# Kernel tuning notes

Measured on AMD Instinct MI355X. Metric: run time of the kernel, lower is better.

## Reference

```python
import jax, jax.numpy as jnp
import numpy as np

N_NODES = 60000
N_EDGES = 960000
IN_C = 128
HID = 4 * IN_C       # 512
D_CAT = 8 * IN_C     # 1024
D_FC = 16 * IN_C     # 2048
D_L1 = 32 * IN_C     # 4096
OUT_C = 64
BN_EPS = 1e-5
LEAKY_SLOPE = 0.01


def setup_inputs() -> dict:
    key = jax.random.key(0)
    ks = jax.random.split(key, 32)
    d = {}
    d['x'] = jax.random.normal(ks[0], (N_NODES, IN_C), dtype=jnp.float32)
    d['edge_index'] = jax.random.randint(ks[1], (2, N_EDGES), 0, N_NODES, dtype=jnp.int64)

    def lin(k, fan_in, fan_out):
        k1, k2 = jax.random.split(k)
        bound = 1.0 / np.sqrt(fan_in)
        w = jax.random.uniform(k1, (fan_in, fan_out), jnp.float32, -bound, bound)
        b = jax.random.uniform(k2, (fan_out,), jnp.float32, -bound, bound)
        return w, b

    # GIN conv A MLP: Linear(IN_C,HID) -> BN(HID) -> ReLU -> Linear(HID,HID) -> ReLU
    d['w1a'], d['b1a'] = lin(ks[2], IN_C, HID)
    d['gamma_a'] = jnp.ones((HID,), jnp.float32)
    d['beta_a'] = jnp.zeros((HID,), jnp.float32)
    d['mean_a'] = jax.random.normal(ks[3], (HID,), jnp.float32) * 0.1
    d['var_a'] = jax.random.uniform(ks[4], (HID,), jnp.float32, 0.5, 1.5)
    d['w2a'], d['b2a'] = lin(ks[5], HID, HID)
    # GIN conv B MLP
    d['w1b'], d['b1b'] = lin(ks[6], IN_C, HID)
    d['gamma_b'] = jnp.ones((HID,), jnp.float32)
    d['beta_b'] = jnp.zeros((HID,), jnp.float32)
    d['mean_b'] = jax.random.normal(ks[7], (HID,), jnp.float32) * 0.1
    d['var_b'] = jax.random.uniform(ks[8], (HID,), jnp.float32, 0.5, 1.5)
    d['w2b'], d['b2b'] = lin(ks[9], HID, HID)
    # dense head
    d['fc_w'], d['fc_b'] = lin(ks[10], D_CAT, D_FC)
    d['l1_w'], d['l1_b'] = lin(ks[11], D_FC, D_L1)
    d['l2_w'], d['l2_b'] = lin(ks[12], D_L1, D_FC)
    d['out_w'], d['out_b'] = lin(ks[13], D_FC, OUT_C)
    return d


def _gin_conv(x, edge_index, w1, b1, gamma, beta, mean, var, w2, b2):
    # GINConv, eps=0: h_i = MLP(x_i + sum_{j->i} x_j)
    src, dst = edge_index[0], edge_index[1]
    agg = jax.ops.segment_sum(x[src], dst, num_segments=x.shape[0])
    h = x + agg
    h = h @ w1 + b1
    # BatchNorm1d in eval mode (running stats)
    h = (h - mean) * jax.lax.rsqrt(var + BN_EPS) * gamma + beta
    h = jax.nn.relu(h)
    h = jax.nn.relu(h @ w2 + b2)
    return h


def reference(x, edge_index, w1a, b1a, gamma_a, beta_a, mean_a, var_a, w2a, b2a,
              w1b, b1b, gamma_b, beta_b, mean_b, var_b, w2b, b2b,
              fc_w, fc_b, l1_w, l1_b, l2_w, l2_b, out_w, out_b):
    x1 = _gin_conv(x, edge_index, w1a, b1a, gamma_a, beta_a, mean_a, var_a, w2a, b2a)
    x2 = _gin_conv(x, edge_index, w1b, b1b, gamma_b, beta_b, mean_b, var_b, w2b, b2b)
    h = jnp.concatenate([x1, x2], axis=1)               # [N, 8*in]
    h = jax.nn.leaky_relu(h @ fc_w + fc_b, LEAKY_SLOPE)  # dropout is identity in eval
    h = h @ l1_w + l1_b
    h = h @ l2_w + l2_b
    h = jax.nn.sigmoid(h @ out_w + out_b)
    return h
```

## Files before the change

### kernel.cpp

```cpp
#include <hip/hip_runtime.h>


#define NN 60000
#define NE 960000
#define C_IN 128
#define HID 512
#define DCAT 1024
#define DFC 2048
#define DL1 4096
#define OUTC 64

typedef __bf16 bf16x8 __attribute__((ext_vector_type(8)));
typedef float floatx4 __attribute__((ext_vector_type(4)));

__device__ __forceinline__ unsigned short f2b(float f) {
  unsigned int u = __float_as_uint(f);
  unsigned int r = (u + 0x7fffu + ((u >> 16) & 1u)) >> 16;
  return (unsigned short)r;
}

#define GLOAD_LDS16(g, l)                                                     \
  __builtin_amdgcn_global_load_lds(                                           \
      (__attribute__((address_space(1))) void*)(g),                           \
      (__attribute__((address_space(3))) void*)(l), 16, 0, 0)

__global__ void k_bnparams(const float* __restrict__ g,
                           const float* __restrict__ be,
                           const float* __restrict__ mn,
                           const float* __restrict__ vr,
                           const float* __restrict__ b1,
                           float* __restrict__ scale, float* __restrict__ shift) {
  int i = blockIdx.x * 256 + threadIdx.x;
  if (i < HID) {
    float s = g[i] * rsqrtf(vr[i] + 1e-5f);
    scale[i] = s;
    shift[i] = (b1[i] - mn[i]) * s + be[i];
  }
}

__global__ void k_transpose(const float* __restrict__ in,
                            unsigned short* __restrict__ out, int K, int N) {
  __shared__ float t[32][33];
  int n0 = blockIdx.x * 32, k0 = blockIdx.y * 32;
  int tx = threadIdx.x & 31, ty = threadIdx.x >> 5;
#pragma unroll
  for (int i = 0; i < 32; i += 8)
    t[ty + i][tx] = in[(size_t)(k0 + ty + i) * N + n0 + tx];
  __syncthreads();
#pragma unroll
  for (int i = 0; i < 32; i += 8)
    out[(size_t)(n0 + ty + i) * K + k0 + tx] = f2b(t[tx][ty + i]);
}

__global__ void k_deg(const int* __restrict__ dst, int* __restrict__ deg) {
  int e = blockIdx.x * 256 + threadIdx.x;
  if (e < NE) atomicAdd(&deg[dst[e]], 1);
}

__global__ void k_scan1(const int* __restrict__ deg, int* __restrict__ offs,
                        int* __restrict__ bsum) {
  __shared__ int t[256];
  int i = blockIdx.x * 256 + threadIdx.x;
  int v = (i < NN) ? deg[i] : 0;
  t[threadIdx.x] = v;
  __syncthreads();
#pragma unroll
  for (int d = 1; d < 256; d <<= 1) {
    int add = (threadIdx.x >= d) ? t[threadIdx.x - d] : 0;
    __syncthreads();
    t[threadIdx.x] += add;
    __syncthreads();
  }
  if (i < NN) offs[i] = t[threadIdx.x] - v;
  if (threadIdx.x == 255) bsum[blockIdx.x] = t[255];
}

__global__ void k_scan2(int* __restrict__ bsum, int nb) {
  __shared__ int t[256];
  int v = (threadIdx.x < nb) ? bsum[threadIdx.x] : 0;
  t[threadIdx.x] = v;
  __syncthreads();
#pragma unroll
  for (int d = 1; d < 256; d <<= 1) {
    int add = (threadIdx.x >= d) ? t[threadIdx.x - d] : 0;
    __syncthreads();
    t[threadIdx.x] += add;
    __syncthreads();
  }
  if (threadIdx.x < nb) bsum[threadIdx.x] = t[threadIdx.x] - v;
}

__global__ void k_scan3(int* __restrict__ offs, const int* __restrict__ bsum,
                        int* __restrict__ cursor) {
  int i = blockIdx.x * 256 + threadIdx.x;
  if (i < NN) {
    int o = offs[i] + bsum[blockIdx.x];
    offs[i] = o;
    cursor[i] = o;
  }
  if (i == 0) offs[NN] = NE;
}

__global__ void k_bucket(const int* __restrict__ src, const int* __restrict__ dst,
                         int* __restrict__ cursor, int* __restrict__ esrc) {
  int e = blockIdx.x * 256 + threadIdx.x;
  if (e < NE) {
    int slot = atomicAdd(&cursor[dst[e]], 1);
    esrc[slot] = src[e];
  }
}

__global__ void k_agg(const float2* __restrict__ x2, const int* __restrict__ offs,
                      const int* __restrict__ esrc, unsigned int* __restrict__ h0u) {
  int node = blockIdx.x * 4 + (threadIdx.x >> 6);
  if (node >= NN) return;
  int lane = threadIdx.x & 63;
  int beg = offs[node], end = offs[node + 1];
  float2 acc = x2[(size_t)node * 64 + lane];
  for (int j = beg; j < end; j++) {
    int s = esrc[j];
    float2 v = x2[(size_t)s * 64 + lane];
    acc.x += v.x;
    acc.y += v.y;
  }
  h0u[(size_t)node * 64 + lane] =
      (unsigned)f2b(acc.x) | ((unsigned)f2b(acc.y) << 16);
}

template <int EPI>
__device__ __forceinline__ void gemm_epilogue(
    floatx4 (&acc)[8][4], unsigned short* C, const float* bias,
    const float* scale, const float* shift, int M, int N, int ldc, int m0,
    int n0, int w, int quad, int r16) {
#pragma unroll
  for (int j = 0; j < 4; j++) {
    int gn = n0 + w * 64 + j * 16 + r16;
    int cn = gn < N ? gn : 0;
    float p0, p1 = 0.f;
    if constexpr (EPI == 2) {
      p0 = scale[cn];
      p1 = shift[cn];
    } else {
      p0 = bias[cn];
    }
#pragma unroll
    for (int i = 0; i < 8; i++) {
#pragma unroll
      for (int t = 0; t < 4; t++) {
        int gm = m0 + i * 16 + quad * 4 + t;
        if (gm < M && gn < N) {
          float v = acc[i][j][t];
          if constexpr (EPI == 0) {
            v += p0;
            C[(size_t)gm * ldc + gn] = f2b(v);
          } else if constexpr (EPI == 1) {
            v += p0; v = v > 0.f ? v : 0.f;
            C[(size_t)gm * ldc + gn] = f2b(v);
          } else if constexpr (EPI == 2) {
            v = v * p0 + p1; v = v > 0.f ? v : 0.f;
            C[(size_t)gm * ldc + gn] = f2b(v);
          } else if constexpr (EPI == 3) {
            v += p0; v = v > 0.f ? v : 0.01f * v;
            C[(size_t)gm * ldc + gn] = f2b(v);
          } else {
            v += p0;
            v = 1.f / (1.f + __expf(-v));
            ((float*)C)[(size_t)gm * ldc + gn] = v;
          }
        }
      }
    }
  }
}

__device__ __forceinline__ void gemm_swizzle(int M, int N, int& m0, int& n0) {
  const int mt_total = (M + 127) >> 7, nt_total = (N + 255) >> 8;
  int mt, nt;
  if ((nt_total & 7) == 0) {
    const int ntpx = nt_total >> 3;
    const int x = blockIdx.x & 7;
    const int s = blockIdx.x >> 3;
    nt = x * ntpx + (s % ntpx);
    mt = s / ntpx;
  } else {
    const int GM = 8;
    const int full = (mt_total / GM) * GM;
    const int boundary = full * nt_total;
    int id = blockIdx.x;
    if (id < boundary) {
      int per_group = GM * nt_total;
      int g = id / per_group, r = id % per_group;
      mt = g * GM + r % GM;
      nt = r / GM;
    } else {
      int r = id - boundary, gm = mt_total - full;
      mt = full + r % gm;
      nt = r / gm;
    }
  }
  m0 = mt << 7;
  n0 = nt << 8;
}

__device__ __forceinline__ void gemm_swizzle256(int M, int N, int& m0, int& n0) {
  const int mt_total = (M + 255) >> 8, nt_total = N >> 8;
  int mt, nt;
  if ((nt_total & 7) == 0) {
    const int ntpx = nt_total >> 3;
    const int x = blockIdx.x & 7;
    const int s = blockIdx.x >> 3;
    nt = x * ntpx + (s % ntpx);
    mt = s / ntpx;
  } else {
    const int GM = 8;
    const int full = (mt_total / GM) * GM;
    const int boundary = full * nt_total;
    int id = blockIdx.x;
    if (id < boundary) {
      int per_group = GM * nt_total;
      int g = id / per_group, r = id % per_group;
      mt = g * GM + r % GM;
      nt = r / GM;
    } else {
      int r = id - boundary, gm = mt_total - full;
      mt = full + r % gm;
      nt = r / gm;
    }
  }
  m0 = mt << 8;
  n0 = nt << 8;
}

template <int EPI>
__global__ __launch_bounds__(256, 2) void k_gemm_g(
    const unsigned short* __restrict__ A, const unsigned short* __restrict__ Bt,
    unsigned short* __restrict__ C, const float* __restrict__ bias,
    const float* __restrict__ scale, const float* __restrict__ shift,
    int M, int N, int K, int lda, int ldc) {
  __shared__ __align__(16) unsigned short lsA[4][4][128][8];

  const int tid = threadIdx.x;
  const int w = tid >> 6;
  const int lane = tid & 63;
  const int quad = lane >> 4;
  const int r16 = lane & 15;

  int m0, n0;
  gemm_swizzle(M, N, m0, n0);

  const int ra0 = min(m0 + lane, M - 1);
  const int ra1 = min(m0 + 64 + lane, M - 1);
  const unsigned short* pA0 = A + (size_t)ra0 * lda + w * 8;
  const unsigned short* pA1 = A + (size_t)ra1 * lda + w * 8;
  const unsigned short* pB[4];
#pragma unroll
  for (int j = 0; j < 4; j++) {
    int rb = min(n0 + w * 64 + j * 16 + r16, N - 1);
    pB[j] = Bt + (size_t)rb * K + quad * 8;
  }

  floatx4 acc[8][4];
#pragma unroll
  for (int i = 0; i < 8; i++)
#pragma unroll
    for (int j = 0; j < 4; j++) acc[i][j] = (floatx4){0.f, 0.f, 0.f, 0.f};

  const int niter = K >> 5;

#define ISSUE_A(st)                                                           \
  do {                                                                        \
    GLOAD_LDS16(pA0, &lsA[st][w][0][0]);                                      \
    GLOAD_LDS16(pA1, &lsA[st][w][64][0]);                                     \
    pA0 += 32; pA1 += 32;                                                     \
  } while (0)

  ISSUE_A(0);
  if (niter > 1) ISSUE_A(1);
  if (niter > 2) ISSUE_A(2);
  bf16x8 bcur[4], bnxt[4];
#pragma unroll
  for (int j = 0; j < 4; j++) {
    bcur[j] = *(const bf16x8*)pB[j];
    pB[j] += 32;
  }

  int st = 0;
  for (int t = 0; t < niter; t++) {
    if (t + 2 < niter) {
      asm volatile("s_waitcnt vmcnt(8)\n\ts_barrier" ::: "memory");
    } else if (t + 1 < niter) {
      asm volatile("s_waitcnt vmcnt(6)\n\ts_barrier" ::: "memory");
    } else {
      asm volatile("s_waitcnt vmcnt(4)\n\ts_barrier" ::: "memory");
    }
    if (t + 3 < niter) {
      int s3 = st + 3;
      if (s3 >= 4) s3 -= 4;
      ISSUE_A(s3);
    }
    if (t + 1 < niter) {
#pragma unroll
      for (int j = 0; j < 4; j++) {
        bnxt[j] = *(const bf16x8*)pB[j];
        pB[j] += 32;
      }
    }

    bf16x8 af[8];
#pragma unroll
    for (int i = 0; i < 8; i++)
      af[i] = *(const bf16x8*)&lsA[st][quad][i * 16 + r16][0];
#pragma unroll
    for (int j = 0; j < 4; j++)
#pragma unroll
      for (int i = 0; i < 8; i++)
        acc[i][j] = __builtin_amdgcn_mfma_f32_16x16x32_bf16(af[i], bcur[j],
                                                            acc[i][j], 0, 0, 0);
#pragma unroll
    for (int j = 0; j < 4; j++) bcur[j] = bnxt[j];
    st = (st + 1) & 3;
  }
#undef ISSUE_A

  gemm_epilogue<EPI>(acc, C, bias, scale, shift, M, N, ldc, m0, n0, w, quad, r16);
}

template <int EPI>
__global__ __launch_bounds__(512, 2) void k_gemm8(
    const unsigned short* __restrict__ A, const unsigned short* __restrict__ Bt,
    unsigned short* __restrict__ C, const float* __restrict__ bias,
    const float* __restrict__ scale, const float* __restrict__ shift,
    int M, int N, int K, int lda, int ldc) {
  __shared__ __align__(16) unsigned short smem[2][2][256][64];

  const int tid = threadIdx.x;
  const int w = tid >> 6;
  const int lane = tid & 63;
  const int wm = w >> 2;
  const int wn = w & 3;
  const int quad = lane >> 4;
  const int r16 = lane & 15;

  int m0, n0;
  gemm_swizzle256(M, N, m0, n0);

  const int w8l = w * 8 + (lane >> 3);
  const int csrc = (lane & 7) ^ ((lane >> 3) & 7);
  unsigned offA[2][2], offB[2][2];
#pragma unroll
  for (int h = 0; h < 2; h++)
#pragma unroll
    for (int q = 0; q < 2; q++) {
      int ra = m0 + h * 128 + q * 64 + w8l;
      ra = ra < M ? ra : (M - 1);
      offA[h][q] = (unsigned)ra * (unsigned)(lda * 2) + (unsigned)(csrc * 16);
      int rb = n0 + h * 128 + q * 64 + w8l;
      offB[h][q] = (unsigned)rb * (unsigned)(K * 2) + (unsigned)(csrc * 16);
    }
  const char* Ac = (const char*)A;
  const char* Bc = (const char*)Bt;
  char* smc = (char*)smem;
  const unsigned wdst = (unsigned)(w * 1024);

#define STG_A(T_, h_)                                                          \
  do {                                                                         \
    unsigned kb_ = (unsigned)(T_) * 128u;                                      \
    unsigned db_ = (unsigned)(((T_) & 1) << 16) + (unsigned)((h_) * 16384) + wdst; \
    GLOAD_LDS16(Ac + offA[h_][0] + kb_, smc + db_);                            \
    GLOAD_LDS16(Ac + offA[h_][1] + kb_, smc + db_ + 8192u);                    \
  } while (0)
#define STG_B(T_, h_)                                                          \
  do {                                                                         \
    unsigned kb_ = (unsigned)(T_) * 128u;                                      \
    unsigned db_ = (unsigned)(((T_) & 1) << 16) + 32768u +                     \
                   (unsigned)((h_) * 16384) + wdst;                            \
    GLOAD_LDS16(Bc + offB[h_][0] + kb_, smc + db_);                            \
    GLOAD_LDS16(Bc + offB[h_][1] + kb_, smc + db_ + 8192u);                    \
  } while (0)

  const int swz = r16 & 7;
  const unsigned cK0 = (unsigned)(((quad) ^ swz) * 16);
  const unsigned cK1 = (unsigned)(((4 + quad) ^ swz) * 16);
  const unsigned rdA = (unsigned)((wm * 128 + r16) * 128);
  const unsigned rdB = 32768u + (unsigned)((wn * 64 + r16) * 128);

#define RD_A(bo_, i_, c_) (*(const bf16x8*)(smc + (bo_) + rdA + (unsigned)((i_)*2048) + (c_)))
#define RD_B(bo_, j_, c_) (*(const bf16x8*)(smc + (bo_) + rdB + (unsigned)((j_)*2048) + (c_)))

  floatx4 acc[8][4];
#pragma unroll
  for (int i = 0; i < 8; i++)
#pragma unroll
    for (int j = 0; j < 4; j++) acc[i][j] = (floatx4){0.f, 0.f, 0.f, 0.f};

  const int NT = K >> 6;

#define MM2(i0_, AF)                                                          \
  do {                                                                        \
    __builtin_amdgcn_s_setprio(1);                                            \
    _Pragma("unroll")                                                         \
    for (int jj = 0; jj < 4; jj++) {                                          \
      acc[(i0_)][jj] = __builtin_amdgcn_mfma_f32_16x16x32_bf16(               \
          AF[0][0], bF[jj][0], acc[(i0_)][jj], 0, 0, 0);                      \
      acc[(i0_)][jj] = __builtin_amdgcn_mfma_f32_16x16x32_bf16(               \
          AF[0][1], bF[jj][1], acc[(i0_)][jj], 0, 0, 0);                      \
      acc[(i0_) + 1][jj] = __builtin_amdgcn_mfma_f32_16x16x32_bf16(           \
          AF[1][0], bF[jj][0], acc[(i0_) + 1][jj], 0, 0, 0);                  \
      acc[(i0_) + 1][jj] = __builtin_amdgcn_mfma_f32_16x16x32_bf16(           \
          AF[1][1], bF[jj][1], acc[(i0_) + 1][jj], 0, 0, 0);                  \
    }                                                                         \
    __builtin_amdgcn_s_setprio(0);                                            \
  } while (0)

  STG_A(0, 0); STG_A(0, 1); STG_B(0, 0); STG_B(0, 1);
  asm volatile("s_waitcnt vmcnt(0)\n\ts_barrier" ::: "memory");

  bf16x8 bF[4][2], aP[2][2], aQ[2][2];

  for (int T = 0; T < NT; T++) {
    const unsigned bo = (unsigned)((T & 1) << 16);
#pragma unroll
    for (int j = 0; j < 4; j++) { bF[j][0] = RD_B(bo, j, cK0); bF[j][1] = RD_B(bo, j, cK1); }
    aP[0][0] = RD_A(bo, 0, cK0); aP[0][1] = RD_A(bo, 0, cK1);
    aP[1][0] = RD_A(bo, 1, cK0); aP[1][1] = RD_A(bo, 1, cK1);
    if (T + 1 < NT) { STG_A(T + 1, 0); STG_A(T + 1, 1); STG_B(T + 1, 0); STG_B(T + 1, 1); }
    aQ[0][0] = RD_A(bo, 2, cK0); aQ[0][1] = RD_A(bo, 2, cK1);
    aQ[1][0] = RD_A(bo, 3, cK0); aQ[1][1] = RD_A(bo, 3, cK1);
    MM2(0, aP);
    aP[0][0] = RD_A(bo, 4, cK0); aP[0][1] = RD_A(bo, 4, cK1);
    aP[1][0] = RD_A(bo, 5, cK0); aP[1][1] = RD_A(bo, 5, cK1);
    MM2(2, aQ);
    aQ[0][0] = RD_A(bo, 6, cK0); aQ[0][1] = RD_A(bo, 6, cK1);
    aQ[1][0] = RD_A(bo, 7, cK0); aQ[1][1] = RD_A(bo, 7, cK1);
    MM2(4, aP);
    MM2(6, aQ);
    if (T + 1 < NT) {
      asm volatile("s_waitcnt vmcnt(0)\n\ts_barrier" ::: "memory");
    }
  }
#undef MM2
#undef STG_A
#undef STG_B
#undef RD_A
#undef RD_B

  __syncthreads();
  char* eb = smc + (unsigned)(w * 16384);
#pragma unroll
  for (int j = 0; j < 4; j++) {
    int gn = n0 + wn * 64 + j * 16 + r16;
    float p0 = 0.f, p1 = 0.f;
    if constexpr (EPI == 2) {
      p0 = scale[gn];
      p1 = shift[gn];
    } else {
      p0 = bias[gn];
    }
#pragma unroll
    for (int i = 0; i < 8; i++)
#pragma unroll
      for (int t = 0; t < 4; t++) {
        float v = acc[i][j][t];
        if constexpr (EPI == 0) {
          v += p0;
        } else if constexpr (EPI == 1) {
          v += p0; v = v > 0.f ? v : 0.f;
        } else if constexpr (EPI == 2) {
          v = v * p0 + p1; v = v > 0.f ? v : 0.f;
        } else {
          v += p0; v = v > 0.f ? v : 0.01f * v;
        }
        int row = i * 16 + quad * 4 + t;
        int col = j * 16 + r16;
        *(unsigned short*)(eb + row * 128 + (((col >> 3) ^ (row & 7)) << 4) +
                           ((col & 7) << 1)) = f2b(v);
      }
  }
#pragma unroll
  for (int r8 = 0; r8 < 16; r8++) {
    int row = r8 * 8 + (lane >> 3);
    int chunkG = lane & 7;
    bf16x8 vv = *(const bf16x8*)(eb + row * 128 + ((chunkG ^ (lane >> 3)) << 4));
    int gm = m0 + wm * 128 + row;
    if (gm < M)
      *(bf16x8*)(C + (size_t)gm * ldc + (n0 + wn * 64 + chunkG * 8)) = vv;
  }
}

extern "C" void kernel_launch(void* const* d_in, const int* in_sizes, int n_in,
                              void* d_out, int out_size, void* d_ws,
                              size_t ws_size, hipStream_t stream) {
  typedef const float* cf;
  cf x = (cf)d_in[0];
  const int* ei = (const int*)d_in[1];
  const int* srcI = ei;
  const int* dstI = ei + NE;
  cf w1a = (cf)d_in[2],  b1a = (cf)d_in[3];
  cf ga = (cf)d_in[4],   bea = (cf)d_in[5];
  cf mna = (cf)d_in[6],  vra = (cf)d_in[7];
  cf w2a = (cf)d_in[8],  b2a = (cf)d_in[9];
  cf w1b = (cf)d_in[10], b1b = (cf)d_in[11];
  cf gb = (cf)d_in[12],  beb = (cf)d_in[13];
  cf mnb = (cf)d_in[14], vrb = (cf)d_in[15];
  cf w2b = (cf)d_in[16], b2b = (cf)d_in[17];
  cf fc_w = (cf)d_in[18], fc_b = (cf)d_in[19];
  cf l1_w = (cf)d_in[20], l1_b = (cf)d_in[21];
  cf l2_w = (cf)d_in[22], l2_b = (cf)d_in[23];
  cf ow = (cf)d_in[24],   ob = (cf)d_in[25];
  float* outf = (float*)d_out;

  char* ws = (char*)d_ws;
  size_t off = 0;
  auto carve = [&](size_t bytes) {
    void* p = ws + off;
    off += (bytes + 255) & ~(size_t)255;
    return p;
  };
  unsigned short* wt1ab = (unsigned short*)carve((size_t)DCAT * C_IN * 2);
  unsigned short* wt2a = (unsigned short*)carve((size_t)HID * HID * 2);
  unsigned short* wt2b = (unsigned short*)carve((size_t)HID * HID * 2);
  unsigned short* wtfc = (unsigned short*)carve((size_t)DFC * DCAT * 2);
  unsigned short* wtl1 = (unsigned short*)carve((size_t)DL1 * DFC * 2);
  unsigned short* wtl2 = (unsigned short*)carve((size_t)DFC * DL1 * 2);
  unsigned short* wtout = (unsigned short*)carve((size_t)OUTC * DFC * 2);
  float* scale_ab = (float*)carve(DCAT * 4);
  float* shift_ab = (float*)carve(DCAT * 4);
  unsigned short* h0 = (unsigned short*)carve((size_t)NN * C_IN * 2);

  size_t off_overlay = off;
  int* deg = (int*)carve((size_t)NN * 4);
  int* offs = (int*)carve((size_t)(NN + 1) * 4);
  int* cursor = (int*)carve((size_t)NN * 4);
  int* bsum = (int*)carve(256 * 4);
  int* esrc = (int*)carve((size_t)NE * 4);

  off = off_overlay;
  size_t rem = (ws_size > off + 4096) ? (ws_size - off - 4096) : 0;
  int mchunk = (int)(rem / ((DFC + DL1) * 2));
  if (mchunk > 15104) mchunk = 15104;
  mchunk &= ~127;
  if (mchunk < 128) mchunk = 128;
  unsigned short* bufA = (unsigned short*)carve((size_t)mchunk * DFC * 2);
  unsigned short* bufB = (unsigned short*)carve((size_t)mchunk * DL1 * 2);
  (void)in_sizes; (void)n_in; (void)out_size;

  k_bnparams<<<2, 256, 0, stream>>>(ga, bea, mna, vra, b1a, scale_ab, shift_ab);
  k_bnparams<<<2, 256, 0, stream>>>(gb, beb, mnb, vrb, b1b, scale_ab + HID,
                                    shift_ab + HID);
  k_transpose<<<dim3(HID / 32, C_IN / 32), 256, 0, stream>>>(w1a, wt1ab, C_IN, HID);
  k_transpose<<<dim3(HID / 32, C_IN / 32), 256, 0, stream>>>(
      w1b, wt1ab + (size_t)HID * C_IN, C_IN, HID);
  k_transpose<<<dim3(HID / 32, HID / 32), 256, 0, stream>>>(w2a, wt2a, HID, HID);
  k_transpose<<<dim3(HID / 32, HID / 32), 256, 0, stream>>>(w2b, wt2b, HID, HID);
  k_transpose<<<dim3(DFC / 32, DCAT / 32), 256, 0, stream>>>(fc_w, wtfc, DCAT, DFC);
  k_transpose<<<dim3(DL1 / 32, DFC / 32), 256, 0, stream>>>(l1_w, wtl1, DFC, DL1);
  k_transpose<<<dim3(DFC / 32, DL1 / 32), 256, 0, stream>>>(l2_w, wtl2, DL1, DFC);
  k_transpose<<<dim3(OUTC / 32, DFC / 32), 256, 0, stream>>>(ow, wtout, DFC, OUTC);

  const int NB_NODE = (NN + 255) / 256;
  hipMemsetAsync(deg, 0, (size_t)NN * 4, stream);
  k_deg<<<(NE + 255) / 256, 256, 0, stream>>>(dstI, deg);
  k_scan1<<<NB_NODE, 256, 0, stream>>>(deg, offs, bsum);
  k_scan2<<<1, 256, 0, stream>>>(bsum, NB_NODE);
  k_scan3<<<NB_NODE, 256, 0, stream>>>(offs, bsum, cursor);
  k_bucket<<<(NE + 255) / 256, 256, 0, stream>>>(srcI, dstI, cursor, esrc);
  k_agg<<<(NN + 3) / 4, 256, 0, stream>>>((const float2*)x, offs, esrc,
                                          (unsigned int*)h0);

  auto gemm = [&](int var, int epi, const unsigned short* A,
                  const unsigned short* Bt, unsigned short* Cp, cf bias,
                  const float* sc, const float* sh, int M, int N, int K,
                  int lda, int ldc) {
    if (var == 2) {
      dim3 g(((M + 255) / 256) * (N / 256));
      switch (epi) {
        case 0: k_gemm8<0><<<g, 512, 0, stream>>>(A, Bt, Cp, bias, sc, sh, M, N, K, lda, ldc); break;
        default: k_gemm8<3><<<g, 512, 0, stream>>>(A, Bt, Cp, bias, sc, sh, M, N, K, lda, ldc); break;
      }
    } else {
      dim3 g(((M + 127) / 128) * ((N + 255) / 256));
      switch (epi) {
        case 0: k_gemm_g<0><<<g, 256, 0, stream>>>(A, Bt, Cp, bias, sc, sh, M, N, K, lda, ldc); break;
        case 1: k_gemm_g<1><<<g, 256, 0, stream>>>(A, Bt, Cp, bias, sc, sh, M, N, K, lda, ldc); break;
        case 2: k_gemm_g<2><<<g, 256, 0, stream>>>(A, Bt, Cp, bias, sc, sh, M, N, K, lda, ldc); break;
        case 3: k_gemm_g<3><<<g, 256, 0, stream>>>(A, Bt, Cp, bias, sc, sh, M, N, K, lda, ldc); break;
        default: k_gemm_g<4><<<g, 256, 0, stream>>>(A, Bt, Cp, bias, sc, sh, M, N, K, lda, ldc); break;
      }
    }
  };

  for (int m0 = 0; m0 < NN; m0 += mchunk) {
    const int M = (NN - m0 < mchunk) ? (NN - m0) : mchunk;
    const unsigned short* h0c = h0 + (size_t)m0 * C_IN;
    unsigned short* outc = (unsigned short*)(outf + (size_t)m0 * OUTC);
    gemm(1, 2, h0c, wt1ab, bufA, nullptr, scale_ab, shift_ab, M, DCAT, C_IN, C_IN, DCAT);
    gemm(1, 1, bufA, wt2a, bufB, b2a, nullptr, nullptr, M, HID, HID, DCAT, DCAT);
    gemm(1, 1, bufA + HID, wt2b, bufB + HID, b2b, nullptr, nullptr, M, HID, HID, DCAT, DCAT);
    gemm(2, 3, bufB, wtfc, bufA, fc_b, nullptr, nullptr, M, DFC, DCAT, DCAT, DFC);
    gemm(2, 0, bufA, wtl1, bufB, l1_b, nullptr, nullptr, M, DL1, DFC, DFC, DL1);
    gemm(2, 0, bufB, wtl2, bufA, l2_b, nullptr, nullptr, M, DFC, DL1, DL1, DFC);
    gemm(1, 4, bufA, wtout, outc, ob, nullptr, nullptr, M, OUTC, DFC, DFC, OUTC);
  }
}
```

Before: 3.151 ms.

## Add 4-stage BK32 LDS pipeline GEMM variant for fc and l2 layers

Adds a new 256x256-tile bf16 MFMA GEMM kernel that uses a four-deep ring of 32-wide K slices in shared memory. It issues direct global-to-LDS loads two slices ahead and interleaves LDS fragment reads with MFMA batches under raised wave priority. The fc and l2 layers switch to this kernel while l1 keeps the old one. The intent is to hide global load latency and reduce barrier stalls. The cost is 128KB of shared memory per block with 2 blocks per CU requested, which may limit occupancy or fail to fit.

```diff
diff --git a/kernel.cpp b/kernel.cpp
--- a/kernel.cpp
+++ b/kernel.cpp
@@ -487,6 +487,163 @@
   }
 }
 
+template <int EPI>
+__global__ __launch_bounds__(512, 2) void k_gemm8b(
+    const unsigned short* __restrict__ A, const unsigned short* __restrict__ Bt,
+    unsigned short* __restrict__ C, const float* __restrict__ bias,
+    const float* __restrict__ scale, const float* __restrict__ shift,
+    int M, int N, int K, int lda, int ldc) {
+  __shared__ __align__(16) unsigned short smem[4][2][256][32];
+
+  const int tid = threadIdx.x;
+  const int w = tid >> 6;
+  const int lane = tid & 63;
+  const int wm = w >> 2;
+  const int wn = w & 3;
+  const int quad = lane >> 4;
+  const int r16 = lane & 15;
+
+  int m0, n0;
+  gemm_swizzle256(M, N, m0, n0);
+
+  const int w16l = w * 16 + (lane >> 2);
+  const int csrc = (lane & 3) ^ ((lane >> 3) & 3);
+  unsigned offA[2], offB[2];
+#pragma unroll
+  for (int h = 0; h < 2; h++) {
+    int ra = m0 + h * 128 + w16l;
+    ra = ra < M ? ra : (M - 1);
+    offA[h] = (unsigned)ra * (unsigned)(lda * 2) + (unsigned)(csrc * 16);
+    int rb = n0 + h * 128 + w16l;
+    offB[h] = (unsigned)rb * (unsigned)(K * 2) + (unsigned)(csrc * 16);
+  }
+  const char* Ac = (const char*)A;
+  const char* Bc = (const char*)Bt;
+  char* smc = (char*)smem;
+  const unsigned wdst = (unsigned)(w * 1024);
+
+#define STG32(T_)                                                             \
+  do {                                                                        \
+    unsigned kb_ = (unsigned)(T_) * 64u;                                      \
+    unsigned db_ = (unsigned)(((T_) & 3) * 32768) + wdst;                     \
+    GLOAD_LDS16(Ac + offA[0] + kb_, smc + db_);                               \
+    GLOAD_LDS16(Ac + offA[1] + kb_, smc + db_ + 8192u);                       \
+    GLOAD_LDS16(Bc + offB[0] + kb_, smc + db_ + 16384u);                      \
+    GLOAD_LDS16(Bc + offB[1] + kb_, smc + db_ + 24576u);                      \
+  } while (0)
+
+  const unsigned cKq = (unsigned)(((quad ^ ((r16 >> 1) & 3)) & 3) * 16);
+  const unsigned rdA = (unsigned)((wm * 128 + r16) * 64) + cKq;
+  const unsigned rdB = 16384u + (unsigned)((wn * 64 + r16) * 64) + cKq;
+
+#define RD_A32(so_, i_) (*(const bf16x8*)(smc + (so_) + rdA + (unsigned)((i_)*1024)))
+#define RD_B32(so_, j_) (*(const bf16x8*)(smc + (so_) + rdB + (unsigned)((j_)*1024)))
+
+  floatx4 acc[8][4];
+#pragma unroll
+  for (int i = 0; i < 8; i++)
+#pragma unroll
+    for (int j = 0; j < 4; j++) acc[i][j] = (floatx4){0.f, 0.f, 0.f, 0.f};
+
+  const int NT = K >> 5;
+  const int NP = NT >> 1;
+
+#define MM1(i0_, AF, BF)                                                      \
+  do {                                                                        \
+    __builtin_amdgcn_s_setprio(1);                                            \
+    _Pragma("unroll")                                                         \
+    for (int jj = 0; jj < 4; jj++) {                                          \
+      acc[(i0_)][jj] = __builtin_amdgcn_mfma_f32_16x16x32_bf16(               \
+          AF[0], BF[jj], acc[(i0_)][jj], 0, 0, 0);                            \
+      acc[(i0_) + 1][jj] = __builtin_amdgcn_mfma_f32_16x16x32_bf16(           \
+          AF[1], BF[jj], acc[(i0_) + 1][jj], 0, 0, 0);                        \
+    }                                                                         \
+    __builtin_amdgcn_s_setprio(0);                                            \
+  } while (0)
+
+  STG32(0);
+  STG32(1);
+  asm volatile("s_waitcnt vmcnt(0)\n\ts_barrier" ::: "memory");
+
+  bf16x8 bF[4], bG[4], aX[2], aY[2];
+
+  for (int p = 0; p < NP; p++) {
+    const int t0 = 2 * p, t1 = 2 * p + 1;
+    const unsigned so0 = (unsigned)((t0 & 3) * 32768);
+    const unsigned so1 = (unsigned)((t1 & 3) * 32768);
+#pragma unroll
+    for (int j = 0; j < 4; j++) bF[j] = RD_B32(so0, j);
+    aX[0] = RD_A32(so0, 0); aX[1] = RD_A32(so0, 1);
+    if (p + 1 < NP) { STG32(t0 + 2); STG32(t1 + 2); }
+    aY[0] = RD_A32(so0, 2); aY[1] = RD_A32(so0, 3);
+    MM1(0, aX, bF);
+    aX[0] = RD_A32(so0, 4); aX[1] = RD_A32(so0, 5);
+    MM1(2, aY, bF);
+    aY[0] = RD_A32(so0, 6); aY[1] = RD_A32(so0, 7);
+    MM1(4, aX, bF);
+#pragma unroll
+    for (int j = 0; j < 4; j++) bG[j] = RD_B32(so1, j);
+    aX[0] = RD_A32(so1, 0); aX[1] = RD_A32(so1, 1);
+    MM1(6, aY, bF);
+    aY[0] = RD_A32(so1, 2); aY[1] = RD_A32(so1, 3);
+    MM1(0, aX, bG);
+    aX[0] = RD_A32(so1, 4); aX[1] = RD_A32(so1, 5);
+    MM1(2, aY, bG);
+    aY[0] = RD_A32(so1, 6); aY[1] = RD_A32(so1, 7);
+    MM1(4, aX, bG);
+    MM1(6, aY, bG);
+    if (p + 1 < NP) {
+      asm volatile("s_waitcnt vmcnt(0)\n\ts_barrier" ::: "memory");
+    }
+  }
+#undef MM1
+#undef STG32
+#undef RD_A32
+#undef RD_B32
+
+  __syncthreads();
+  char* eb = smc + (unsigned)(w * 16384);
+#pragma unroll
+  for (int j = 0; j < 4; j++) {
+    int gn = n0 + wn * 64 + j * 16 + r16;
+    float p0 = 0.f, p1 = 0.f;
+    if constexpr (EPI == 2) {
+      p0 = scale[gn];
+      p1 = shift[gn];
+    } else {
+      p0 = bias[gn];
+    }
+#pragma unroll
+    for (int i = 0; i < 8; i++)
+#pragma unroll
+      for (int t = 0; t < 4; t++) {
+        float v = acc[i][j][t];
+        if constexpr (EPI == 0) {
+          v += p0;
+        } else if constexpr (EPI == 1) {
+          v += p0; v = v > 0.f ? v : 0.f;
+        } else if constexpr (EPI == 2) {
+          v = v * p0 + p1; v = v > 0.f ? v : 0.f;
+        } else {
+          v += p0; v = v > 0.f ? v : 0.01f * v;
+        }
+        int row = i * 16 + quad * 4 + t;
+        int col = j * 16 + r16;
+        *(unsigned short*)(eb + row * 128 + (((col >> 3) ^ (row & 7)) << 4) +
+                           ((col & 7) << 1)) = f2b(v);
+      }
+  }
+#pragma unroll
+  for (int r8 = 0; r8 < 16; r8++) {
+    int row = r8 * 8 + (lane >> 3);
+    int chunkG = lane & 7;
+    bf16x8 vv = *(const bf16x8*)(eb + row * 128 + ((chunkG ^ (lane >> 3)) << 4));
+    int gm = m0 + wm * 128 + row;
+    if (gm < M)
+      *(bf16x8*)(C + (size_t)gm * ldc + (n0 + wn * 64 + chunkG * 8)) = vv;
+  }
+}
+
 extern "C" void kernel_launch(void* const* d_in, const int* in_sizes, int n_in,
                               void* d_out, int out_size, void* d_ws,
                               size_t ws_size, hipStream_t stream) {
@@ -577,6 +734,12 @@
         case 0: k_gemm8<0><<<g, 512, 0, stream>>>(A, Bt, Cp, bias, sc, sh, M, N, K, lda, ldc); break;
         default: k_gemm8<3><<<g, 512, 0, stream>>>(A, Bt, Cp, bias, sc, sh, M, N, K, lda, ldc); break;
       }
+    } else if (var == 3) {
+      dim3 g(((M + 255) / 256) * (N / 256));
+      switch (epi) {
+        case 0: k_gemm8b<0><<<g, 512, 0, stream>>>(A, Bt, Cp, bias, sc, sh, M, N, K, lda, ldc); break;
+        default: k_gemm8b<3><<<g, 512, 0, stream>>>(A, Bt, Cp, bias, sc, sh, M, N, K, lda, ldc); break;
+      }
     } else {
       dim3 g(((M + 127) / 128) * ((N + 255) / 256));
       switch (epi) {
@@ -596,9 +759,9 @@
     gemm(1, 2, h0c, wt1ab, bufA, nullptr, scale_ab, shift_ab, M, DCAT, C_IN, C_IN, DCAT);
     gemm(1, 1, bufA, wt2a, bufB, b2a, nullptr, nullptr, M, HID, HID, DCAT, DCAT);
     gemm(1, 1, bufA + HID, wt2b, bufB + HID, b2b, nullptr, nullptr, M, HID, HID, DCAT, DCAT);
-    gemm(2, 3, bufB, wtfc, bufA, fc_b, nullptr, nullptr, M, DFC, DCAT, DCAT, DFC);
+    gemm(3, 3, bufB, wtfc, bufA, fc_b, nullptr, nullptr, M, DFC, DCAT, DCAT, DFC);
     gemm(2, 0, bufA, wtl1, bufB, l1_b, nullptr, nullptr, M, DL1, DFC, DFC, DL1);
-    gemm(2, 0, bufB, wtl2, bufA, l2_b, nullptr, nullptr, M, DFC, DL1, DL1, DFC);
+    gemm(3, 0, bufB, wtl2, bufA, l2_b, nullptr, nullptr, M, DFC, DL1, DL1, DFC);
     gemm(1, 4, bufA, wtout, outc, ob, nullptr, nullptr, M, OUTC, DFC, DFC, OUTC);
   }
 }
```

Measured after the change: 3.184 ms. Within noise of the previous version (+1.0%).
